# Kernel optimization log

Measured on AMD Instinct MI355X. Metric: run time of the kernel, lower is better.

## Reference

```python
import jax, jax.numpy as jnp
import numpy as np

N_IN, N_H, N_OUT = 256, 2048, 256
BATCH, T = 64, 512


def setup_inputs() -> dict:
    key = jax.random.key(0)
    k_u, k_uh, k_hh, k_hy, k_h0 = jax.random.split(key, 5)
    u = jax.random.normal(k_u, (BATCH, T, N_IN), dtype=jnp.float32)
    # sparse_normal_weights with p=1: N(0, g^2/N_src), returned transposed -> (N_src, N_dst)
    W_uh = jax.random.normal(k_uh, (N_IN, N_H), dtype=jnp.float32) / np.sqrt(N_IN)
    W_hh = jax.random.normal(k_hh, (N_H, N_H), dtype=jnp.float32) / np.sqrt(N_H)
    W_hy = jax.random.normal(k_hy, (N_H, N_OUT), dtype=jnp.float32) / np.sqrt(N_H)
    b_h = jnp.zeros((N_H,), dtype=jnp.float32)
    b_y = jnp.zeros((N_OUT,), dtype=jnp.float32)
    # h0 ~ Uniform[-1, 1] (tanh branch)
    h0 = jax.random.uniform(k_h0, (N_H,), dtype=jnp.float32, minval=-1.0, maxval=1.0)
    tau = jnp.ones((N_H,), dtype=jnp.float32)
    return {"u": u, "W_uh": W_uh, "W_hh": W_hh, "W_hy": W_hy,
            "b_h": b_h, "b_y": b_y, "h0": h0, "tau": tau}


def reference(u, W_uh, W_hh, W_hy, b_h, b_y, h0, tau):
    # Leaky CTRNN, f_h=tanh, f_out=softmax, noise=0.0, h0=None path
    alpha = 1.0 / tau                      # (N_h,)
    h0c = jnp.clip(h0, -1.0, 1.0)          # clip_initial_state for tanh
    batch = u.shape[0]
    h_init = jnp.broadcast_to(h0c, (batch, N_H))

    def step(h, u_t):
        pre = h @ W_hh + u_t @ W_uh + b_h          # (B, N_h)
        h_new = (1.0 - alpha) * h + alpha * jnp.tanh(pre)
        y_t = jax.nn.softmax(h_new @ W_hy + b_y, axis=1)  # (B, N_out)
        return h_new, y_t

    u_t_first = jnp.swapaxes(u, 0, 1)              # (T, B, N_in)
    _, y = jax.lax.scan(step, h_init, u_t_first)   # y: (T, B, N_out)
    return jnp.swapaxes(y, 0, 1)                   # (B, T, N_out)
```

## Files before the change

### kernel.cpp

```cpp
#include <hip/hip_runtime.h>
#include <hip/hip_fp16.h>

#define N_INP 256
#define NH    2048
#define NOUT  256
#define BB    64
#define TT    512
#define GRIDN 128
#define NWAVE (GRIDN * 4)

typedef __bf16 bf16x8 __attribute__((ext_vector_type(8)));
typedef float  f32x4  __attribute__((ext_vector_type(4)));

__device__ __forceinline__ unsigned short f2bf(float f) {
  unsigned u = __float_as_uint(f);
  u += 0x7fffu + ((u >> 16) & 1u);
  return (unsigned short)(u >> 16);
}

__device__ __forceinline__ float fast_tanh(float x) {
  x = fminf(9.0f, fmaxf(-9.0f, x));
  float e = __expf(2.0f * x);
  return (e - 1.0f) / (e + 1.0f);
}

__device__ __forceinline__ f32x4 mfma16(uint4 a, uint4 b, f32x4 c) {
  return __builtin_amdgcn_mfma_f32_16x16x32_bf16(
      __builtin_bit_cast(bf16x8, a), __builtin_bit_cast(bf16x8, b), c, 0, 0, 0);
}

__device__ __forceinline__ void bar_arrive(unsigned* __restrict__ flags, int s,
                                           int waveid, int lane) {
  __builtin_amdgcn_fence(__ATOMIC_RELEASE, "workgroup");
  if (lane == 0)
    __hip_atomic_store(flags + (size_t)s * NWAVE + waveid, 1u,
                       __ATOMIC_RELAXED, __HIP_MEMORY_SCOPE_AGENT);
}

__device__ __forceinline__ void bar_wait(unsigned* __restrict__ flags, int s,
                                         int wave, int lane, unsigned* bar_cnt) {
  if (wave == 0) {
    const unsigned* f = flags + (size_t)s * NWAVE;
    for (;;) {
      unsigned ok = 1u;
#pragma unroll
      for (int j = 0; j < 8; ++j) {
        unsigned v = __hip_atomic_load(f + j * 64 + lane, __ATOMIC_RELAXED,
                                       __HIP_MEMORY_SCOPE_AGENT);
        ok &= (v != 0u) ? 1u : 0u;
      }
      if (__all(ok)) break;
    }
    __hip_atomic_store(bar_cnt, (unsigned)(s + 1), __ATOMIC_RELAXED,
                       __HIP_MEMORY_SCOPE_WORKGROUP);
  } else {
    while (__hip_atomic_load(bar_cnt, __ATOMIC_RELAXED,
                             __HIP_MEMORY_SCOPE_WORKGROUP) < (unsigned)(s + 1))
      __builtin_amdgcn_s_sleep(1);
  }
  __builtin_amdgcn_fence(__ATOMIC_ACQUIRE, "workgroup");
}

__global__ void k_zero(unsigned* __restrict__ p, int n) {
  int i = blockIdx.x * 256 + threadIdx.x;
  if (i < n) p[i] = 0;
}

__global__ void k_ut(const float* __restrict__ u, unsigned short* __restrict__ ut) {
  int idx = blockIdx.x * 256 + threadIdx.x;
  int k4 = idx & 63;
  int rowbt = idx >> 6;
  int t = rowbt >> 6, b = rowbt & 63;
  float4 f = *(const float4*)(u + ((size_t)b * TT + t) * N_INP + k4 * 4);
  uint2 pk;
  pk.x = f2bf(f.x) | ((unsigned)f2bf(f.y) << 16);
  pk.y = f2bf(f.z) | ((unsigned)f2bf(f.w) << 16);
  *(uint2*)(ut + (size_t)rowbt * N_INP + k4 * 4) = pk;
}

__global__ void k_swz(const float* __restrict__ W, unsigned short* __restrict__ Wf, int N) {
  int lane = threadIdx.x;
  int nt16 = N >> 4;
  int kb = blockIdx.x / nt16;
  int nt = blockIdx.x - kb * nt16;
  int k0 = kb * 32 + ((lane >> 4) << 3);
  int c  = nt * 16 + (lane & 15);
  unsigned short v[8];
#pragma unroll
  for (int j = 0; j < 8; ++j) v[j] = f2bf(W[(size_t)(k0 + j) * N + c]);
  uint4 p;
  p.x = v[0] | ((unsigned)v[1] << 16);
  p.y = v[2] | ((unsigned)v[3] << 16);
  p.z = v[4] | ((unsigned)v[5] << 16);
  p.w = v[6] | ((unsigned)v[7] << 16);
  ((uint4*)Wf)[(size_t)blockIdx.x * 64 + lane] = p;
}

__global__ __launch_bounds__(256) void k_step(
    const float* __restrict__ Whh, const float* __restrict__ Wuh,
    const float* __restrict__ b_h, const float* __restrict__ tau,
    const float* __restrict__ h0, const unsigned short* __restrict__ ut,
    unsigned short* __restrict__ H, unsigned* __restrict__ flags) {
  __shared__ unsigned short lds[64 * 64 * 8];
  __shared__ unsigned bar_cnt;
  const int cgp = blockIdx.x;
  const int tid = threadIdx.x;
  const int wave = tid >> 6;
  const int lane = tid & 63;
  const int q = lane >> 4, p = lane & 15;
  const int waveid = cgp * 4 + wave;

  for (int s = tid; s < 64 * 64; s += 256) {
    int kb = s >> 6, l = s & 63;
    int k0 = kb * 32 + ((l >> 4) << 3);
    int c = cgp * 16 + (l & 15);
    unsigned short v[8];
#pragma unroll
    for (int j = 0; j < 8; ++j) v[j] = f2bf(Whh[(size_t)(k0 + j) * NH + c]);
    uint4 pk;
    pk.x = v[0] | ((unsigned)v[1] << 16);
    pk.y = v[2] | ((unsigned)v[3] << 16);
    pk.z = v[4] | ((unsigned)v[5] << 16);
    pk.w = v[6] | ((unsigned)v[7] << 16);
    ((uint4*)lds)[s] = pk;
  }
  if (tid == 0) bar_cnt = 0;

  const int c = cgp * 16 + p;
  const float al = 1.0f / tau[c];
  const float onem = 1.0f - al;
  const float bh_c = b_h[c];
  const float h0c = fminf(1.0f, fmaxf(-1.0f, h0[c]));
  float hprev[4] = {h0c, h0c, h0c, h0c};
  const int rbase = wave * 16;
  const bool even = (p & 1) == 0;
  const int halfc = cgp * 8 + (p >> 1);
  unsigned* H32 = (unsigned*)H;

  uint4 wu[8];
#pragma unroll
  for (int kb = 0; kb < 8; ++kb) {
    unsigned short v[8];
#pragma unroll
    for (int j = 0; j < 8; ++j)
      v[j] = f2bf(Wuh[(size_t)(kb * 32 + q * 8 + j) * NH + c]);
    wu[kb].x = v[0] | ((unsigned)v[1] << 16);
    wu[kb].y = v[2] | ((unsigned)v[3] << 16);
    wu[kb].z = v[4] | ((unsigned)v[5] << 16);
    wu[kb].w = v[6] | ((unsigned)v[7] << 16);
  }

  __syncthreads();

  {
    unsigned mine = f2bf(h0c);
    unsigned other = (unsigned)__shfl_xor((int)mine, 1);
    unsigned pk0 = even ? (mine | (other << 16)) : (other | (mine << 16));
    if (even) {
#pragma unroll
      for (int r = 0; r < 4; ++r)
        __hip_atomic_store(H32 + (size_t)(rbase + q * 4 + r) * (NH / 2) + halfc,
                           pk0, __ATOMIC_RELAXED, __HIP_MEMORY_SCOPE_AGENT);
    }
  }

  const uint4* ldsv = (const uint4*)lds;
  f32x4 acc[4];

  bar_arrive(flags, 0, waveid, lane);
  {
    const uint4* Au = (const uint4*)(ut + ((size_t)(rbase + p)) * N_INP + q * 8);
#pragma unroll
    for (int j = 0; j < 4; ++j) acc[j] = (f32x4){0.f, 0.f, 0.f, 0.f};
#pragma unroll
    for (int kb = 0; kb < 8; ++kb)
      acc[kb & 3] = mfma16(Au[kb * 4], wu[kb], acc[kb & 3]);
  }
  bar_wait(flags, 0, wave, lane, &bar_cnt);

  for (int t = 0; t < TT; ++t) {
    const uint4* Ar = (const uint4*)(H + (size_t)t * BB * NH + (size_t)(rbase + p) * NH + q * 8);
    uint4 a[8];
#pragma unroll
    for (int j = 0; j < 8; ++j) a[j] = Ar[j * 4];
#pragma unroll
    for (int kb = 0; kb < 64; kb += 8) {
      uint4 an[8];
      if (kb < 56) {
#pragma unroll
        for (int j = 0; j < 8; ++j) an[j] = Ar[(kb + 8 + j) * 4];
      }
#pragma unroll
      for (int j = 0; j < 8; ++j)
        acc[j & 3] = mfma16(a[j], ldsv[(kb + j) * 64 + lane], acc[j & 3]);
      if (kb < 56) {
#pragma unroll
        for (int j = 0; j < 8; ++j) a[j] = an[j];
      }
    }

    unsigned* H32n = H32 + (size_t)(t + 1) * BB * (NH / 2);
#pragma unroll
    for (int r = 0; r < 4; ++r) {
      float pre = acc[0][r] + acc[1][r] + acc[2][r] + acc[3][r] + bh_c;
      float hn = onem * hprev[r] + al * fast_tanh(pre);
      hprev[r] = hn;
      unsigned mine = f2bf(hn);
      unsigned other = (unsigned)__shfl_xor((int)mine, 1);
      unsigned pk = even ? (mine | (other << 16)) : (other | (mine << 16));
      if (even)
        __hip_atomic_store(H32n + (size_t)(rbase + q * 4 + r) * (NH / 2) + halfc,
                           pk, __ATOMIC_RELAXED, __HIP_MEMORY_SCOPE_AGENT);
    }

    if (t + 1 < TT) {
      bar_arrive(flags, t + 1, waveid, lane);
      const uint4* Au = (const uint4*)(ut + ((size_t)(t + 1) * BB + rbase + p) * N_INP + q * 8);
#pragma unroll
      for (int j = 0; j < 4; ++j) acc[j] = (f32x4){0.f, 0.f, 0.f, 0.f};
#pragma unroll
      for (int kb = 0; kb < 8; ++kb)
        acc[kb & 3] = mfma16(Au[kb * 4], wu[kb], acc[kb & 3]);
      bar_wait(flags, t + 1, wave, lane, &bar_cnt);
    }
  }
}

__global__ __launch_bounds__(256) void k_y(
    const unsigned short* __restrict__ H, const unsigned short* __restrict__ Wyf,
    const float* __restrict__ b_y, float* __restrict__ out) {
  int wave = threadIdx.x >> 6, lane = threadIdx.x & 63;
  int q = lane >> 4, p = lane & 15;
  int R = blockIdx.x * 64 + wave * 16;
  const uint4* A = (const uint4*)(H + (size_t)(R + BB + p) * NH + q * 8);
  const uint4* Bf = (const uint4*)Wyf;
  f32x4 acc[16];
#pragma unroll
  for (int nt = 0; nt < 16; ++nt) acc[nt] = (f32x4){0.f, 0.f, 0.f, 0.f};
  for (int kb = 0; kb < 64; ++kb) {
    uint4 a = A[kb * 4];
#pragma unroll
    for (int nt = 0; nt < 16; ++nt) {
      uint4 b = Bf[(size_t)(kb * 16 + nt) * 64 + lane];
      acc[nt] = mfma16(a, b, acc[nt]);
    }
  }
  float bb[16];
#pragma unroll
  for (int nt = 0; nt < 16; ++nt) bb[nt] = b_y[nt * 16 + p];
#pragma unroll
  for (int r = 0; r < 4; ++r) {
    int row = R + q * 4 + r;
    int tI = row >> 6, bI = row & 63;
    float lg[16];
    float mx = -1e30f;
#pragma unroll
    for (int nt = 0; nt < 16; ++nt) { lg[nt] = acc[nt][r] + bb[nt]; mx = fmaxf(mx, lg[nt]); }
#pragma unroll
    for (int d = 1; d < 16; d <<= 1) mx = fmaxf(mx, __shfl_xor(mx, d));
    float s = 0.f;
#pragma unroll
    for (int nt = 0; nt < 16; ++nt) { lg[nt] = __expf(lg[nt] - mx); s += lg[nt]; }
#pragma unroll
    for (int d = 1; d < 16; d <<= 1) s += __shfl_xor(s, d);
    float inv = 1.0f / s;
    float* orow = out + ((size_t)bI * TT + tI) * NOUT;
#pragma unroll
    for (int nt = 0; nt < 16; ++nt) orow[nt * 16 + p] = lg[nt] * inv;
  }
}

extern "C" void kernel_launch(void* const* d_in, const int* in_sizes, int n_in,
                              void* d_out, int out_size, void* d_ws, size_t ws_size,
                              hipStream_t stream) {
  (void)in_sizes; (void)n_in; (void)out_size; (void)ws_size;
  const float* u   = (const float*)d_in[0];
  const float* Wuh = (const float*)d_in[1];
  const float* Whh = (const float*)d_in[2];
  const float* Why = (const float*)d_in[3];
  const float* b_h = (const float*)d_in[4];
  const float* b_y = (const float*)d_in[5];
  const float* h0  = (const float*)d_in[6];
  const float* tau = (const float*)d_in[7];
  float* out = (float*)d_out;

  char* ws = (char*)d_ws;
  unsigned short* H = (unsigned short*)ws;
  size_t off = (size_t)(TT + 1) * BB * NH * 2;
  unsigned short* ut = (unsigned short*)(ws + off);
  off += (size_t)TT * BB * N_INP * 2;
  unsigned short* Wyf = (unsigned short*)(ws + off);
  off += (size_t)NH * NOUT * 2;
  unsigned* flags = (unsigned*)(ws + off);

  const int nz = (TT + 1) * NWAVE;
  k_zero<<<dim3((nz + 255) / 256), dim3(256), 0, stream>>>(flags, nz);
  k_ut<<<dim3(8192), dim3(256), 0, stream>>>(u, ut);
  k_swz<<<dim3((NH / 32) * (NOUT / 16)), dim3(64), 0, stream>>>(Why, Wyf, NOUT);

  void* args[] = {(void*)&Whh, (void*)&Wuh, (void*)&b_h, (void*)&tau,
                  (void*)&h0, (void*)&ut, (void*)&H, (void*)&flags};
  hipLaunchCooperativeKernel((const void*)k_step, dim3(GRIDN), dim3(256), args, 0, stream);

  k_y<<<dim3(512), dim3(256), 0, stream>>>(H, Wyf, b_y, out);
}
```

Before: 4.871 ms.

## Halve step-kernel grid, widen column tiles, use per-wave row-group flag barriers

Cuts the persistent recurrence kernel from 128 to 64 workgroups, each owning 32 hidden columns, with W_hh and W_uh staged in LDS. The global barrier changes: each wave now waits only on flags from the 64 waves that produce its own 16 batch rows, polled by a single ballot, with no workgroup-level counter. This is meant to lower barrier fan-in and latency per timestep and to reuse each loaded H fragment for two column tiles. The costs are fewer CUs doing the matmul work, 64 uint4 registers holding A fragments (pressure and possible spills), and a new flag layout that relies on the host zeroing flags for all timesteps.

```diff
diff --git a/kernel.cpp b/kernel.cpp
--- a/kernel.cpp
+++ b/kernel.cpp
@@ -6,7 +6,7 @@
 #define NOUT  256
 #define BB    64
 #define TT    512
-#define GRIDN 128
+#define GRIDN 64
 #define NWAVE (GRIDN * 4)
 
 typedef __bf16 bf16x8 __attribute__((ext_vector_type(8)));
@@ -27,38 +27,6 @@
 __device__ __forceinline__ f32x4 mfma16(uint4 a, uint4 b, f32x4 c) {
   return __builtin_amdgcn_mfma_f32_16x16x32_bf16(
       __builtin_bit_cast(bf16x8, a), __builtin_bit_cast(bf16x8, b), c, 0, 0, 0);
-}
-
-__device__ __forceinline__ void bar_arrive(unsigned* __restrict__ flags, int s,
-                                           int waveid, int lane) {
-  __builtin_amdgcn_fence(__ATOMIC_RELEASE, "workgroup");
-  if (lane == 0)
-    __hip_atomic_store(flags + (size_t)s * NWAVE + waveid, 1u,
-                       __ATOMIC_RELAXED, __HIP_MEMORY_SCOPE_AGENT);
-}
-
-__device__ __forceinline__ void bar_wait(unsigned* __restrict__ flags, int s,
-                                         int wave, int lane, unsigned* bar_cnt) {
-  if (wave == 0) {
-    const unsigned* f = flags + (size_t)s * NWAVE;
-    for (;;) {
-      unsigned ok = 1u;
-#pragma unroll
-      for (int j = 0; j < 8; ++j) {
-        unsigned v = __hip_atomic_load(f + j * 64 + lane, __ATOMIC_RELAXED,
-                                       __HIP_MEMORY_SCOPE_AGENT);
-        ok &= (v != 0u) ? 1u : 0u;
-      }
-      if (__all(ok)) break;
-    }
-    __hip_atomic_store(bar_cnt, (unsigned)(s + 1), __ATOMIC_RELAXED,
-                       __HIP_MEMORY_SCOPE_WORKGROUP);
-  } else {
-    while (__hip_atomic_load(bar_cnt, __ATOMIC_RELAXED,
-                             __HIP_MEMORY_SCOPE_WORKGROUP) < (unsigned)(s + 1))
-      __builtin_amdgcn_s_sleep(1);
-  }
-  __builtin_amdgcn_fence(__ATOMIC_ACQUIRE, "workgroup");
 }
 
 __global__ void k_zero(unsigned* __restrict__ p, int n) {
@@ -96,24 +64,23 @@
   ((uint4*)Wf)[(size_t)blockIdx.x * 64 + lane] = p;
 }
 
-__global__ __launch_bounds__(256) void k_step(
+__global__ __launch_bounds__(256, 1) void k_step(
     const float* __restrict__ Whh, const float* __restrict__ Wuh,
     const float* __restrict__ b_h, const float* __restrict__ tau,
     const float* __restrict__ h0, const unsigned short* __restrict__ ut,
     unsigned short* __restrict__ H, unsigned* __restrict__ flags) {
-  __shared__ unsigned short lds[64 * 64 * 8];
-  __shared__ unsigned bar_cnt;
+  __shared__ unsigned short ldsW[64 * 2 * 64 * 8];
+  __shared__ unsigned short ldsU[8 * 2 * 64 * 8];
   const int cgp = blockIdx.x;
   const int tid = threadIdx.x;
   const int wave = tid >> 6;
   const int lane = tid & 63;
   const int q = lane >> 4, p = lane & 15;
-  const int waveid = cgp * 4 + wave;
-
-  for (int s = tid; s < 64 * 64; s += 256) {
-    int kb = s >> 6, l = s & 63;
+
+  for (int s = tid; s < 64 * 2 * 64; s += 256) {
+    int kb = s >> 7, nt = (s >> 6) & 1, l = s & 63;
     int k0 = kb * 32 + ((l >> 4) << 3);
-    int c = cgp * 16 + (l & 15);
+    int c  = cgp * 32 + nt * 16 + (l & 15);
     unsigned short v[8];
 #pragma unroll
     for (int j = 0; j < 8; ++j) v[j] = f2bf(Whh[(size_t)(k0 + j) * NH + c]);
@@ -122,107 +89,138 @@
     pk.y = v[2] | ((unsigned)v[3] << 16);
     pk.z = v[4] | ((unsigned)v[5] << 16);
     pk.w = v[6] | ((unsigned)v[7] << 16);
-    ((uint4*)lds)[s] = pk;
-  }
-  if (tid == 0) bar_cnt = 0;
-
-  const int c = cgp * 16 + p;
-  const float al = 1.0f / tau[c];
-  const float onem = 1.0f - al;
-  const float bh_c = b_h[c];
-  const float h0c = fminf(1.0f, fmaxf(-1.0f, h0[c]));
-  float hprev[4] = {h0c, h0c, h0c, h0c};
+    ((uint4*)ldsW)[s] = pk;
+  }
+  for (int s = tid; s < 8 * 2 * 64; s += 256) {
+    int kb = s >> 7, nt = (s >> 6) & 1, l = s & 63;
+    int k0 = kb * 32 + ((l >> 4) << 3);
+    int c  = cgp * 32 + nt * 16 + (l & 15);
+    unsigned short v[8];
+#pragma unroll
+    for (int j = 0; j < 8; ++j) v[j] = f2bf(Wuh[(size_t)(k0 + j) * NH + c]);
+    uint4 pk;
+    pk.x = v[0] | ((unsigned)v[1] << 16);
+    pk.y = v[2] | ((unsigned)v[3] << 16);
+    pk.z = v[4] | ((unsigned)v[5] << 16);
+    pk.w = v[6] | ((unsigned)v[7] << 16);
+    ((uint4*)ldsU)[s] = pk;
+  }
+
+  const int c0 = cgp * 32 + p, c1 = c0 + 16;
+  const float al0 = 1.0f / tau[c0], al1 = 1.0f / tau[c1];
+  const float onem0 = 1.0f - al0, onem1 = 1.0f - al1;
+  const float bh0 = b_h[c0], bh1 = b_h[c1];
+  const float h00 = fminf(1.0f, fmaxf(-1.0f, h0[c0]));
+  const float h01 = fminf(1.0f, fmaxf(-1.0f, h0[c1]));
+  float hp0[4] = {h00, h00, h00, h00};
+  float hp1[4] = {h01, h01, h01, h01};
   const int rbase = wave * 16;
   const bool even = (p & 1) == 0;
-  const int halfc = cgp * 8 + (p >> 1);
+  const int halfc0 = cgp * 16 + (p >> 1);
+  const int halfc1 = halfc0 + 8;
   unsigned* H32 = (unsigned*)H;
 
-  uint4 wu[8];
-#pragma unroll
-  for (int kb = 0; kb < 8; ++kb) {
-    unsigned short v[8];
-#pragma unroll
-    for (int j = 0; j < 8; ++j)
-      v[j] = f2bf(Wuh[(size_t)(kb * 32 + q * 8 + j) * NH + c]);
-    wu[kb].x = v[0] | ((unsigned)v[1] << 16);
-    wu[kb].y = v[2] | ((unsigned)v[3] << 16);
-    wu[kb].z = v[4] | ((unsigned)v[5] << 16);
-    wu[kb].w = v[6] | ((unsigned)v[7] << 16);
-  }
-
   __syncthreads();
 
   {
-    unsigned mine = f2bf(h0c);
-    unsigned other = (unsigned)__shfl_xor((int)mine, 1);
-    unsigned pk0 = even ? (mine | (other << 16)) : (other | (mine << 16));
+    unsigned m0 = f2bf(h00), m1 = f2bf(h01);
+    unsigned o0 = (unsigned)__shfl_xor((int)m0, 1);
+    unsigned o1 = (unsigned)__shfl_xor((int)m1, 1);
     if (even) {
-#pragma unroll
-      for (int r = 0; r < 4; ++r)
-        __hip_atomic_store(H32 + (size_t)(rbase + q * 4 + r) * (NH / 2) + halfc,
-                           pk0, __ATOMIC_RELAXED, __HIP_MEMORY_SCOPE_AGENT);
-    }
-  }
-
-  const uint4* ldsv = (const uint4*)lds;
-  f32x4 acc[4];
-
-  bar_arrive(flags, 0, waveid, lane);
-  {
-    const uint4* Au = (const uint4*)(ut + ((size_t)(rbase + p)) * N_INP + q * 8);
-#pragma unroll
-    for (int j = 0; j < 4; ++j) acc[j] = (f32x4){0.f, 0.f, 0.f, 0.f};
-#pragma unroll
-    for (int kb = 0; kb < 8; ++kb)
-      acc[kb & 3] = mfma16(Au[kb * 4], wu[kb], acc[kb & 3]);
-  }
-  bar_wait(flags, 0, wave, lane, &bar_cnt);
+      unsigned pk0 = m0 | (o0 << 16);
+      unsigned pk1 = m1 | (o1 << 16);
+#pragma unroll
+      for (int r = 0; r < 4; ++r) {
+        size_t ro = (size_t)(rbase + q * 4 + r) * (NH / 2);
+        __hip_atomic_store(H32 + ro + halfc0, pk0, __ATOMIC_RELAXED,
+                           __HIP_MEMORY_SCOPE_AGENT);
+        __hip_atomic_store(H32 + ro + halfc1, pk1, __ATOMIC_RELAXED,
+                           __HIP_MEMORY_SCOPE_AGENT);
+      }
+    }
+  }
+  __builtin_amdgcn_fence(__ATOMIC_RELEASE, "workgroup");
+  if (lane == 0)
+    __hip_atomic_store(flags + (size_t)wave * 64 + cgp, 1u, __ATOMIC_RELAXED,
+                       __HIP_MEMORY_SCOPE_AGENT);
+
+  const uint4* Wf = (const uint4*)ldsW;
+  const uint4* Uf = (const uint4*)ldsU;
 
   for (int t = 0; t < TT; ++t) {
-    const uint4* Ar = (const uint4*)(H + (size_t)t * BB * NH + (size_t)(rbase + p) * NH + q * 8);
-    uint4 a[8];
-#pragma unroll
-    for (int j = 0; j < 8; ++j) a[j] = Ar[j * 4];
-#pragma unroll
-    for (int kb = 0; kb < 64; kb += 8) {
-      uint4 an[8];
-      if (kb < 56) {
-#pragma unroll
-        for (int j = 0; j < 8; ++j) an[j] = Ar[(kb + 8 + j) * 4];
+    const uint4* Au = (const uint4*)(ut + ((size_t)t * BB + rbase + p) * N_INP + q * 8);
+    uint4 au[8];
+#pragma unroll
+    for (int kb = 0; kb < 8; ++kb) au[kb] = Au[kb * 4];
+
+    f32x4 acc0[4], acc1[4];
+#pragma unroll
+    for (int j = 0; j < 4; ++j) {
+      acc0[j] = (f32x4){0.f, 0.f, 0.f, 0.f};
+      acc1[j] = (f32x4){0.f, 0.f, 0.f, 0.f};
+    }
+
+    const unsigned* fl = flags + (size_t)t * NWAVE + wave * 64;
+    unsigned long long rdy = 0;
+    while (rdy != ~0ull) {
+      unsigned v = __hip_atomic_load(fl + lane, __ATOMIC_RELAXED,
+                                     __HIP_MEMORY_SCOPE_AGENT);
+      rdy = __ballot(v != 0u);
+    }
+    __builtin_amdgcn_fence(__ATOMIC_ACQUIRE, "workgroup");
+
+    const uint4* Ar = (const uint4*)(H + (size_t)t * BB * NH +
+                                     (size_t)(rbase + p) * NH + q * 8);
+    uint4 a[32];
+#pragma unroll
+    for (int j = 0; j < 32; ++j) a[j] = Ar[j * 4];
+
+#pragma unroll
+    for (int kb = 0; kb < 8; ++kb) {
+      acc0[kb & 3] = mfma16(au[kb], Uf[(kb * 2 + 0) * 64 + lane], acc0[kb & 3]);
+      acc1[kb & 3] = mfma16(au[kb], Uf[(kb * 2 + 1) * 64 + lane], acc1[kb & 3]);
+    }
+
+    uint4 an[32];
+#pragma unroll
+    for (int j = 0; j < 32; ++j) an[j] = Ar[(32 + j) * 4];
+
+#pragma unroll
+    for (int j = 0; j < 32; ++j) {
+      acc0[j & 3] = mfma16(a[j], Wf[(j * 2 + 0) * 64 + lane], acc0[j & 3]);
+      acc1[j & 3] = mfma16(a[j], Wf[(j * 2 + 1) * 64 + lane], acc1[j & 3]);
+    }
+#pragma unroll
+    for (int j = 0; j < 32; ++j) {
+      acc0[j & 3] = mfma16(an[j], Wf[((32 + j) * 2 + 0) * 64 + lane], acc0[j & 3]);
+      acc1[j & 3] = mfma16(an[j], Wf[((32 + j) * 2 + 1) * 64 + lane], acc1[j & 3]);
+    }
+
+    unsigned* H32n = H32 + (size_t)(t + 1) * BB * (NH / 2);
+#pragma unroll
+    for (int r = 0; r < 4; ++r) {
+      float pre0 = acc0[0][r] + acc0[1][r] + acc0[2][r] + acc0[3][r] + bh0;
+      float pre1 = acc1[0][r] + acc1[1][r] + acc1[2][r] + acc1[3][r] + bh1;
+      float hn0 = onem0 * hp0[r] + al0 * fast_tanh(pre0);
+      float hn1 = onem1 * hp1[r] + al1 * fast_tanh(pre1);
+      hp0[r] = hn0;
+      hp1[r] = hn1;
+      unsigned m0 = f2bf(hn0), m1 = f2bf(hn1);
+      unsigned o0 = (unsigned)__shfl_xor((int)m0, 1);
+      unsigned o1 = (unsigned)__shfl_xor((int)m1, 1);
+      if (even) {
+        size_t ro = (size_t)(rbase + q * 4 + r) * (NH / 2);
+        __hip_atomic_store(H32n + ro + halfc0, m0 | (o0 << 16),
+                           __ATOMIC_RELAXED, __HIP_MEMORY_SCOPE_AGENT);
+        __hip_atomic_store(H32n + ro + halfc1, m1 | (o1 << 16),
+                           __ATOMIC_RELAXED, __HIP_MEMORY_SCOPE_AGENT);
       }
-#pragma unroll
-      for (int j = 0; j < 8; ++j)
-        acc[j & 3] = mfma16(a[j], ldsv[(kb + j) * 64 + lane], acc[j & 3]);
-      if (kb < 56) {
-#pragma unroll
-        for (int j = 0; j < 8; ++j) a[j] = an[j];
-      }
-    }
-
-    unsigned* H32n = H32 + (size_t)(t + 1) * BB * (NH / 2);
-#pragma unroll
-    for (int r = 0; r < 4; ++r) {
-      float pre = acc[0][r] + acc[1][r] + acc[2][r] + acc[3][r] + bh_c;
-      float hn = onem * hprev[r] + al * fast_tanh(pre);
-      hprev[r] = hn;
-      unsigned mine = f2bf(hn);
-      unsigned other = (unsigned)__shfl_xor((int)mine, 1);
-      unsigned pk = even ? (mine | (other << 16)) : (other | (mine << 16));
-      if (even)
-        __hip_atomic_store(H32n + (size_t)(rbase + q * 4 + r) * (NH / 2) + halfc,
-                           pk, __ATOMIC_RELAXED, __HIP_MEMORY_SCOPE_AGENT);
-    }
-
-    if (t + 1 < TT) {
-      bar_arrive(flags, t + 1, waveid, lane);
-      const uint4* Au = (const uint4*)(ut + ((size_t)(t + 1) * BB + rbase + p) * N_INP + q * 8);
-#pragma unroll
-      for (int j = 0; j < 4; ++j) acc[j] = (f32x4){0.f, 0.f, 0.f, 0.f};
-#pragma unroll
-      for (int kb = 0; kb < 8; ++kb)
-        acc[kb & 3] = mfma16(Au[kb * 4], wu[kb], acc[kb & 3]);
-      bar_wait(flags, t + 1, wave, lane, &bar_cnt);
-    }
+    }
+
+    __builtin_amdgcn_fence(__ATOMIC_RELEASE, "workgroup");
+    if (lane == 0)
+      __hip_atomic_store(flags + (size_t)(t + 1) * NWAVE + wave * 64 + cgp, 1u,
+                         __ATOMIC_RELAXED, __HIP_MEMORY_SCOPE_AGENT);
   }
 }
 
```

Result: slower. 7.997 ms (+64.2%).

## Replace grid-wide per-step barrier with per-row-slice dependency flags

Applied to the files above, without the earlier changes.

Each wave now waits only on the 128 producer waves that write the batch rows it reads (flags indexed by wave slot and block), instead of on all 512 waves through a block-level leader-and-LDS handoff. The per-step barrier becomes a narrower dataflow dependency: each wave polls 128 flags itself, and the input projection is computed before the wait. The aim is to cut barrier latency and the intra-block serialization at every timestep. In exchange, every wave now spin-polls global memory directly, which adds polling traffic.

```diff
diff --git a/kernel.cpp b/kernel.cpp
--- a/kernel.cpp
+++ b/kernel.cpp
@@ -27,38 +27,6 @@
 __device__ __forceinline__ f32x4 mfma16(uint4 a, uint4 b, f32x4 c) {
   return __builtin_amdgcn_mfma_f32_16x16x32_bf16(
       __builtin_bit_cast(bf16x8, a), __builtin_bit_cast(bf16x8, b), c, 0, 0, 0);
-}
-
-__device__ __forceinline__ void bar_arrive(unsigned* __restrict__ flags, int s,
-                                           int waveid, int lane) {
-  __builtin_amdgcn_fence(__ATOMIC_RELEASE, "workgroup");
-  if (lane == 0)
-    __hip_atomic_store(flags + (size_t)s * NWAVE + waveid, 1u,
-                       __ATOMIC_RELAXED, __HIP_MEMORY_SCOPE_AGENT);
-}
-
-__device__ __forceinline__ void bar_wait(unsigned* __restrict__ flags, int s,
-                                         int wave, int lane, unsigned* bar_cnt) {
-  if (wave == 0) {
-    const unsigned* f = flags + (size_t)s * NWAVE;
-    for (;;) {
-      unsigned ok = 1u;
-#pragma unroll
-      for (int j = 0; j < 8; ++j) {
-        unsigned v = __hip_atomic_load(f + j * 64 + lane, __ATOMIC_RELAXED,
-                                       __HIP_MEMORY_SCOPE_AGENT);
-        ok &= (v != 0u) ? 1u : 0u;
-      }
-      if (__all(ok)) break;
-    }
-    __hip_atomic_store(bar_cnt, (unsigned)(s + 1), __ATOMIC_RELAXED,
-                       __HIP_MEMORY_SCOPE_WORKGROUP);
-  } else {
-    while (__hip_atomic_load(bar_cnt, __ATOMIC_RELAXED,
-                             __HIP_MEMORY_SCOPE_WORKGROUP) < (unsigned)(s + 1))
-      __builtin_amdgcn_s_sleep(1);
-  }
-  __builtin_amdgcn_fence(__ATOMIC_ACQUIRE, "workgroup");
 }
 
 __global__ void k_zero(unsigned* __restrict__ p, int n) {
@@ -102,13 +70,11 @@
     const float* __restrict__ h0, const unsigned short* __restrict__ ut,
     unsigned short* __restrict__ H, unsigned* __restrict__ flags) {
   __shared__ unsigned short lds[64 * 64 * 8];
-  __shared__ unsigned bar_cnt;
   const int cgp = blockIdx.x;
   const int tid = threadIdx.x;
   const int wave = tid >> 6;
   const int lane = tid & 63;
   const int q = lane >> 4, p = lane & 15;
-  const int waveid = cgp * 4 + wave;
 
   for (int s = tid; s < 64 * 64; s += 256) {
     int kb = s >> 6, l = s & 63;
@@ -124,7 +90,6 @@
     pk.w = v[6] | ((unsigned)v[7] << 16);
     ((uint4*)lds)[s] = pk;
   }
-  if (tid == 0) bar_cnt = 0;
 
   const int c = cgp * 16 + p;
   const float al = 1.0f / tau[c];
@@ -163,22 +128,34 @@
                            pk0, __ATOMIC_RELAXED, __HIP_MEMORY_SCOPE_AGENT);
     }
   }
+  __builtin_amdgcn_fence(__ATOMIC_RELEASE, "workgroup");
+  if (lane == 0)
+    __hip_atomic_store(flags + (size_t)wave * GRIDN + cgp, 1u, __ATOMIC_RELAXED,
+                       __HIP_MEMORY_SCOPE_AGENT);
 
   const uint4* ldsv = (const uint4*)lds;
   f32x4 acc[4];
 
-  bar_arrive(flags, 0, waveid, lane);
-  {
-    const uint4* Au = (const uint4*)(ut + ((size_t)(rbase + p)) * N_INP + q * 8);
-#pragma unroll
-    for (int j = 0; j < 4; ++j) acc[j] = (f32x4){0.f, 0.f, 0.f, 0.f};
-#pragma unroll
-    for (int kb = 0; kb < 8; ++kb)
-      acc[kb & 3] = mfma16(Au[kb * 4], wu[kb], acc[kb & 3]);
-  }
-  bar_wait(flags, 0, wave, lane, &bar_cnt);
-
   for (int t = 0; t < TT; ++t) {
+    {
+      const uint4* Au = (const uint4*)(ut + ((size_t)t * BB + rbase + p) * N_INP + q * 8);
+#pragma unroll
+      for (int j = 0; j < 4; ++j) acc[j] = (f32x4){0.f, 0.f, 0.f, 0.f};
+#pragma unroll
+      for (int kb = 0; kb < 8; ++kb)
+        acc[kb & 3] = mfma16(Au[kb * 4], wu[kb], acc[kb & 3]);
+    }
+
+    const unsigned* fl = flags + (size_t)t * NWAVE + wave * GRIDN;
+    for (;;) {
+      unsigned v0 = __hip_atomic_load(fl + lane, __ATOMIC_RELAXED,
+                                      __HIP_MEMORY_SCOPE_AGENT);
+      unsigned v1 = __hip_atomic_load(fl + 64 + lane, __ATOMIC_RELAXED,
+                                      __HIP_MEMORY_SCOPE_AGENT);
+      if (__all((v0 != 0u) && (v1 != 0u))) break;
+    }
+    __builtin_amdgcn_fence(__ATOMIC_ACQUIRE, "workgroup");
+
     const uint4* Ar = (const uint4*)(H + (size_t)t * BB * NH + (size_t)(rbase + p) * NH + q * 8);
     uint4 a[8];
 #pragma unroll
@@ -213,16 +190,10 @@
                            pk, __ATOMIC_RELAXED, __HIP_MEMORY_SCOPE_AGENT);
     }
 
-    if (t + 1 < TT) {
-      bar_arrive(flags, t + 1, waveid, lane);
-      const uint4* Au = (const uint4*)(ut + ((size_t)(t + 1) * BB + rbase + p) * N_INP + q * 8);
-#pragma unroll
-      for (int j = 0; j < 4; ++j) acc[j] = (f32x4){0.f, 0.f, 0.f, 0.f};
-#pragma unroll
-      for (int kb = 0; kb < 8; ++kb)
-        acc[kb & 3] = mfma16(Au[kb * 4], wu[kb], acc[kb & 3]);
-      bar_wait(flags, t + 1, wave, lane, &bar_cnt);
-    }
+    __builtin_amdgcn_fence(__ATOMIC_RELEASE, "workgroup");
+    if (lane == 0)
+      __hip_atomic_store(flags + (size_t)(t + 1) * NWAVE + wave * GRIDN + cgp, 1u,
+                         __ATOMIC_RELAXED, __HIP_MEMORY_SCOPE_AGENT);
   }
 }
 
```

New measurement: 4.886 ms. About the same (+0.3%).
